# Kernel tuning notes

Measured on AMD Instinct MI355X. Metric: run time of the kernel, lower is better.

Reference implementation:

```python
import jax, jax.numpy as jnp
import numpy as np

N_S, N_D, E, L = 10000, 2000, 100000, 50000
H = 8            # attention heads
H1, H2, H3 = 128, 128, 64
D_S, D_D = 128, 64
NEG_SLOPE = 0.2  # GATv2 leaky_relu slope


def setup_inputs() -> dict:
    key = jax.random.key(0)
    ks = iter(jax.random.split(key, 48))
    def nrm(shape, fan_in):
        return (jax.random.normal(next(ks), shape) / np.sqrt(fan_in)).astype(jnp.float32)
    inp = {}
    inp["x_snorna"] = jax.random.normal(next(ks), (N_S, D_S), dtype=jnp.float32)
    inp["x_disease"] = jax.random.normal(next(ks), (N_D, D_D), dtype=jnp.float32)
    inp["edge_src"] = jax.random.randint(next(ks), (E,), 0, N_S, dtype=jnp.int32)
    inp["edge_dst"] = jax.random.randint(next(ks), (E,), 0, N_D, dtype=jnp.int32)
    inp["edge_label_src"] = jax.random.randint(next(ks), (L,), 0, N_S, dtype=jnp.int32)
    inp["edge_label_dst"] = jax.random.randint(next(ks), (L,), 0, N_D, dtype=jnp.int32)
    # layer 1: GraphConv per relation (lin_rel has bias, lin_root no bias)
    inp["W1_rel_sd"] = nrm((D_S, H1), D_S); inp["b1_sd"] = jnp.zeros((H1,), jnp.float32)
    inp["W1_root_sd"] = nrm((D_D, H1), D_D)
    inp["W1_rel_ds"] = nrm((D_D, H1), D_D); inp["b1_ds"] = jnp.zeros((H1,), jnp.float32)
    inp["W1_root_ds"] = nrm((D_S, H1), D_S)
    # layer 2: GATv2Conv per relation (lin_l/lin_r with bias, att, final bias)
    for rel in ("sd", "ds"):
        inp[f"Wl2_{rel}"] = nrm((H1, H * H2), H1); inp[f"bl2_{rel}"] = jnp.zeros((H * H2,), jnp.float32)
        inp[f"Wr2_{rel}"] = nrm((H1, H * H2), H1); inp[f"br2_{rel}"] = jnp.zeros((H * H2,), jnp.float32)
        inp[f"att2_{rel}"] = nrm((H, H2), H2)
        inp[f"bias2_{rel}"] = jnp.zeros((H2,), jnp.float32)
    # layer 3: GraphConv per relation
    inp["W3_rel_sd"] = nrm((H2, H3), H2); inp["b3_sd"] = jnp.zeros((H3,), jnp.float32)
    inp["W3_root_sd"] = nrm((H2, H3), H2)
    inp["W3_rel_ds"] = nrm((H2, H3), H2); inp["b3_ds"] = jnp.zeros((H3,), jnp.float32)
    inp["W3_root_ds"] = nrm((H2, H3), H2)
    return inp


def graph_conv(x_src, x_dst, es, ed, W_rel, b_rel, W_root, n_dst):
    # PyG GraphConv: lin_rel(sum-aggregated neighbor feats) + lin_root(x_dst)
    agg = jax.ops.segment_sum(x_src[es], ed, num_segments=n_dst)
    return agg @ W_rel + b_rel + x_dst @ W_root


def gatv2(x_src, x_dst, es, ed, Wl, bl, Wr, br, att, bias, n_dst):
    # PyG GATv2Conv, bipartite, add_self_loops=False, concat=False (mean over heads)
    xl = (x_src @ Wl + bl).reshape(x_src.shape[0], H, -1)  # [Ns,H,C]
    xr = (x_dst @ Wr + br).reshape(x_dst.shape[0], H, -1)  # [Nd,H,C]
    xj = xl[es]                                            # [E,H,C] source msgs
    e = jax.nn.leaky_relu(xj + xr[ed], NEG_SLOPE)          # [E,H,C]
    score = jnp.einsum('ehc,hc->eh', e, att)               # [E,H]
    m = jax.ops.segment_max(score, ed, num_segments=n_dst)
    a = jnp.exp(score - m[ed])
    denom = jax.ops.segment_sum(a, ed, num_segments=n_dst)
    alpha = a / denom[ed]                                  # softmax over in-edges of dst
    out = jax.ops.segment_sum(alpha[:, :, None] * xj, ed, num_segments=n_dst)
    return out.mean(axis=1) + bias                         # concat=False -> head mean


def reference(x_snorna, x_disease, edge_src, edge_dst, edge_label_src, edge_label_dst,
              W1_rel_sd, b1_sd, W1_root_sd, W1_rel_ds, b1_ds, W1_root_ds,
              Wl2_sd, bl2_sd, Wr2_sd, br2_sd, att2_sd, bias2_sd,
              Wl2_ds, bl2_ds, Wr2_ds, br2_ds, att2_ds, bias2_ds,
              W3_rel_sd, b3_sd, W3_root_sd, W3_rel_ds, b3_ds, W3_root_ds):
    # HeteroConv layer 1 (GraphConv both directions); each type has one incoming relation
    xd = graph_conv(x_snorna, x_disease, edge_src, edge_dst, W1_rel_sd, b1_sd, W1_root_sd, N_D)
    xs = graph_conv(x_disease, x_snorna, edge_dst, edge_src, W1_rel_ds, b1_ds, W1_root_ds, N_S)
    xs, xd = jax.nn.relu(xs), jax.nn.relu(xd)  # dropout = identity (eval mode)
    # HeteroConv layer 2 (GATv2Conv both directions)
    xd2 = gatv2(xs, xd, edge_src, edge_dst, Wl2_sd, bl2_sd, Wr2_sd, br2_sd, att2_sd, bias2_sd, N_D)
    xs2 = gatv2(xd, xs, edge_dst, edge_src, Wl2_ds, bl2_ds, Wr2_ds, br2_ds, att2_ds, bias2_ds, N_S)
    xs2, xd2 = jax.nn.relu(xs2), jax.nn.relu(xd2)
    # HeteroConv layer 3 (GraphConv, no activation)
    xd3 = graph_conv(xs2, xd2, edge_src, edge_dst, W3_rel_sd, b3_sd, W3_root_sd, N_D)
    xs3 = graph_conv(xd2, xs2, edge_dst, edge_src, W3_rel_ds, b3_ds, W3_root_ds, N_S)
    # Classifier: per-pair dot product
    return (xs3[edge_label_src] * xd3[edge_label_dst]).sum(axis=-1)
```

## Files before the change

### kernel.cpp

```cpp
#include <hip/hip_runtime.h>
#include <math.h>

#define HH 8
#define C2 128
#define NEG 0.2f

static const int N_S = 10000, N_D = 2000, E_N = 100000, L_N = 50000;

using short8 = __attribute__((ext_vector_type(8))) short;
using f32x4  = __attribute__((ext_vector_type(4))) float;

__device__ inline unsigned short f2bf(float f) {
  unsigned u = __float_as_uint(f);
  u += 0x7fff + ((u >> 16) & 1);
  return (unsigned short)(u >> 16);
}
__device__ inline float bf2f(unsigned short u) {
  return __uint_as_float((unsigned)u << 16);
}
__device__ inline void unpack16(uint4 u0, uint4 u1, float* x) {
  x[0]  = __uint_as_float(u0.x << 16); x[1]  = __uint_as_float(u0.x & 0xffff0000u);
  x[2]  = __uint_as_float(u0.y << 16); x[3]  = __uint_as_float(u0.y & 0xffff0000u);
  x[4]  = __uint_as_float(u0.z << 16); x[5]  = __uint_as_float(u0.z & 0xffff0000u);
  x[6]  = __uint_as_float(u0.w << 16); x[7]  = __uint_as_float(u0.w & 0xffff0000u);
  x[8]  = __uint_as_float(u1.x << 16); x[9]  = __uint_as_float(u1.x & 0xffff0000u);
  x[10] = __uint_as_float(u1.y << 16); x[11] = __uint_as_float(u1.y & 0xffff0000u);
  x[12] = __uint_as_float(u1.z << 16); x[13] = __uint_as_float(u1.z & 0xffff0000u);
  x[14] = __uint_as_float(u1.w << 16); x[15] = __uint_as_float(u1.w & 0xffff0000u);
}

__global__ void k_hist2(const int* __restrict__ es, const int* __restrict__ ed,
                        int* __restrict__ deg_s, int* __restrict__ deg_d, int E) {
  int e = blockIdx.x * 256 + threadIdx.x;
  if (e < E) {
    atomicAdd(&deg_d[ed[e]], 1);
    atomicAdd(&deg_s[es[e]], 1);
  }
}

__global__ __launch_bounds__(1024) void k_scan2(int* c0, int* r0, int n0,
                                                int* c1, int* r1, int n1) {
  int* cur = blockIdx.x ? c1 : c0;
  int* rp  = blockIdx.x ? r1 : r0;
  int N    = blockIdx.x ? n1 : n0;
  __shared__ int wsum[16];
  __shared__ int carry;
  if (threadIdx.x == 0) carry = 0;
  __syncthreads();
  int lane = threadIdx.x & 63, wid = threadIdx.x >> 6;
  for (int base = 0; base < N; base += 1024) {
    int i = base + threadIdx.x;
    int v = (i < N) ? cur[i] : 0;
    int x = v;
    #pragma unroll
    for (int dd = 1; dd < 64; dd <<= 1) {
      int t = __shfl_up(x, dd);
      if (lane >= dd) x += t;
    }
    if (lane == 63) wsum[wid] = x;
    __syncthreads();
    int woff = 0;
    for (int ww = 0; ww < wid; ++ww) woff += wsum[ww];
    int cl = carry;
    int excl = cl + woff + x - v;
    if (i < N) { rp[i] = excl; cur[i] = excl; }
    __syncthreads();
    if (threadIdx.x == 0) {
      int t = 0;
      #pragma unroll
      for (int ww = 0; ww < 16; ++ww) t += wsum[ww];
      if (base + 1024 >= N) rp[N] = carry + t;
      carry += t;
    }
    __syncthreads();
  }
}

__global__ void k_scat2(const int* __restrict__ es, const int* __restrict__ ed,
                        int* __restrict__ cur_d, int* __restrict__ cur_s,
                        int* __restrict__ csrc_d, int* __restrict__ csrc_s, int E) {
  int e = blockIdx.x * 256 + threadIdx.x;
  if (e >= E) return;
  int s = es[e], d = ed[e];
  csrc_d[atomicAdd(&cur_d[d], 1)] = s;
  csrc_s[atomicAdd(&cur_s[s], 1)] = d;
}

__global__ void k_cvt(const float* __restrict__ xs, const float* __restrict__ xd,
                      unsigned short* __restrict__ xsb, unsigned short* __restrict__ xdb) {
  int i = blockIdx.x * 256 + threadIdx.x;
  const int ns4 = N_S * 128 / 4, nd4 = N_D * 64 / 4;
  if (i < ns4) {
    float4 v = ((const float4*)xs)[i];
    ushort4 o = {f2bf(v.x), f2bf(v.y), f2bf(v.z), f2bf(v.w)};
    ((ushort4*)xsb)[i] = o;
  } else if (i < ns4 + nd4) {
    int j = i - ns4;
    float4 v = ((const float4*)xd)[j];
    ushort4 o = {f2bf(v.x), f2bf(v.y), f2bf(v.z), f2bf(v.w)};
    ((ushort4*)xdb)[j] = o;
  }
}

struct PkD { const float* W; unsigned short* P; int K, M; };
struct Pk12 { PkD d[12]; };
__global__ void k_pack(Pk12 g) {
  PkD d = g.d[blockIdx.y];
  int total = d.K * d.M;
  int mt = d.M >> 4;
  for (int tid = blockIdx.x * 256 + threadIdx.x; tid < total; tid += gridDim.x * 256) {
    int r = tid & 7, l = (tid >> 3) & 63;
    int rest = tid >> 9;
    int ct = rest % mt, kt = rest / mt;
    int k = kt * 32 + (l >> 4) * 8 + r;
    int col = ct * 16 + (l & 15);
    d.P[tid] = f2bf(d.W[k * d.M + col]);
  }
}

__global__ __launch_bounds__(128) void k_gather_l1(
    const unsigned short* __restrict__ xsb, const unsigned short* __restrict__ xdb,
    const int* __restrict__ rpd, const int* __restrict__ csd,
    const int* __restrict__ rps, const int* __restrict__ css,
    unsigned short* __restrict__ aggd, unsigned short* __restrict__ aggs) {
  if (blockIdx.x < N_D) {
    int n = blockIdx.x, c = threadIdx.x;
    int b = rpd[n], e = rpd[n + 1];
    float acc = 0.f;
    int i = b;
    for (; i + 1 < e; i += 2)
      acc += bf2f(xsb[(long long)csd[i] * 128 + c]) +
             bf2f(xsb[(long long)csd[i + 1] * 128 + c]);
    if (i < e) acc += bf2f(xsb[(long long)csd[i] * 128 + c]);
    aggd[(long long)n * 128 + c] = f2bf(acc);
  } else {
    int n = (blockIdx.x - N_D) * 2 + (threadIdx.x >> 6);
    int c = threadIdx.x & 63;
    if (n >= N_S) return;
    int b = rps[n], e = rps[n + 1];
    float acc = 0.f;
    int i = b;
    for (; i + 1 < e; i += 2)
      acc += bf2f(xdb[(long long)css[i] * 64 + c]) +
             bf2f(xdb[(long long)css[i + 1] * 64 + c]);
    if (i < e) acc += bf2f(xdb[(long long)css[i] * 64 + c]);
    aggs[(long long)n * 64 + c] = f2bf(acc);
  }
}

__global__ __launch_bounds__(128) void k_gather_l3(
    const unsigned short* __restrict__ xs2b, const unsigned short* __restrict__ xd2b,
    const int* __restrict__ rpd, const int* __restrict__ csd,
    const int* __restrict__ rps, const int* __restrict__ css,
    unsigned short* __restrict__ aggd, unsigned short* __restrict__ aggs) {
  int c = threadIdx.x;
  if (blockIdx.x < N_D) {
    int n = blockIdx.x;
    int b = rpd[n], e = rpd[n + 1];
    float acc = 0.f;
    int i = b;
    for (; i + 1 < e; i += 2)
      acc += bf2f(xs2b[(long long)csd[i] * 128 + c]) +
             bf2f(xs2b[(long long)csd[i + 1] * 128 + c]);
    if (i < e) acc += bf2f(xs2b[(long long)csd[i] * 128 + c]);
    aggd[(long long)n * 128 + c] = f2bf(acc);
  } else {
    int n = blockIdx.x - N_D;
    int b = rps[n], e = rps[n + 1];
    float acc = 0.f;
    int i = b;
    for (; i + 1 < e; i += 2)
      acc += bf2f(xd2b[(long long)css[i] * 128 + c]) +
             bf2f(xd2b[(long long)css[i + 1] * 128 + c]);
    if (i < e) acc += bf2f(xd2b[(long long)css[i] * 128 + c]);
    aggs[(long long)n * 128 + c] = f2bf(acc);
  }
}

struct GD {
  const unsigned short *A0, *P0, *A1, *P1;
  const float* bias;
  void* out;
  int K0, K1, N, M, relu, outbf, y0;
};
template<int ND> struct GDs { GD d[ND]; };

template<int ND>
__global__ __launch_bounds__(256) void k_mfma(GDs<ND> g) {
  int by = blockIdx.y;
  int di = 0;
  #pragma unroll
  for (int i = 1; i < ND; ++i) if (by >= g.d[i].y0) di = i;
  GD d = g.d[di];
  int ytile = by - d.y0;
  int c0 = blockIdx.x * 64;
  if (c0 >= d.M) return;
  int w = threadIdx.x >> 6, l = threadIdx.x & 63;
  int r0 = ytile * 64 + w * 16;
  if (r0 >= d.N) return;
  int lg = l >> 4, lo = l & 15;
  f32x4 acc[4] = {};
  int arow = r0 + lo; arow = (arow < d.N) ? arow : (d.N - 1);
  int mt = d.M >> 4;
  int ct0 = c0 >> 4;
  const unsigned short* a0 = d.A0 + (long long)arow * d.K0 + lg * 8;
  for (int kt = 0; kt < (d.K0 >> 5); ++kt) {
    short8 a = *(const short8*)(a0 + kt * 32);
    #pragma unroll
    for (int ct = 0; ct < 4; ++ct) {
      short8 b = *(const short8*)(d.P0 + ((long long)(kt * mt + ct0 + ct) * 64 + l) * 8);
      acc[ct] = __builtin_amdgcn_mfma_f32_16x16x32_bf16(a, b, acc[ct], 0, 0, 0);
    }
  }
  if (d.K1) {
    const unsigned short* a1 = d.A1 + (long long)arow * d.K1 + lg * 8;
    for (int kt = 0; kt < (d.K1 >> 5); ++kt) {
      short8 a = *(const short8*)(a1 + kt * 32);
      #pragma unroll
      for (int ct = 0; ct < 4; ++ct) {
        short8 b = *(const short8*)(d.P1 + ((long long)(kt * mt + ct0 + ct) * 64 + l) * 8);
        acc[ct] = __builtin_amdgcn_mfma_f32_16x16x32_bf16(a, b, acc[ct], 0, 0, 0);
      }
    }
  }
  #pragma unroll
  for (int ct = 0; ct < 4; ++ct) {
    int col = c0 + ct * 16 + lo;
    float bv = d.bias[col];
    #pragma unroll
    for (int r = 0; r < 4; ++r) {
      int grow = r0 + lg * 4 + r;
      if (grow < d.N) {
        float v = acc[ct][r] + bv;
        if (d.relu) v = fmaxf(v, 0.f);
        if (d.outbf)
          ((unsigned short*)d.out)[(long long)grow * d.M + col] = f2bf(v);
        else
          ((float*)d.out)[(long long)grow * d.M + col] = v;
      }
    }
  }
}

template<int WPN>
__device__ __forceinline__ void gat_node(
    const unsigned short* __restrict__ xl, const unsigned short* __restrict__ xr,
    const int* __restrict__ rowptr, const int* __restrict__ srcid,
    const float* __restrict__ att, const float* __restrict__ bias,
    unsigned short* __restrict__ outb, int node, int wsub, int l,
    float (*lm)[8], float (*lss)[8], float (*lacc)[64][16]) {
  int h = l >> 3, sub = l & 7;
  int cbase = h * 128 + sub * 16;

  float xrv[16], atv[16];
  {
    const uint4* p = (const uint4*)(xr + (long long)node * 1024 + cbase);
    unpack16(p[0], p[1], xrv);
    const float4* pa = (const float4*)(att + cbase);
    float4 a0 = pa[0], a1 = pa[1], a2 = pa[2], a3 = pa[3];
    atv[0] = a0.x; atv[1] = a0.y; atv[2] = a0.z; atv[3] = a0.w;
    atv[4] = a1.x; atv[5] = a1.y; atv[6] = a1.z; atv[7] = a1.w;
    atv[8] = a2.x; atv[9] = a2.y; atv[10] = a2.z; atv[11] = a2.w;
    atv[12] = a3.x; atv[13] = a3.y; atv[14] = a3.z; atv[15] = a3.w;
  }

  float m = -INFINITY, s = 0.f, acc[16] = {};
  int b = rowptr[node], e = rowptr[node + 1];

  auto process = [&](uint4 u0, uint4 u1) {
    float x[16];
    unpack16(u0, u1, x);
    float sc = 0.f;
    #pragma unroll
    for (int j = 0; j < 16; ++j) {
      float t = x[j] + xrv[j];
      t = fmaxf(t, NEG * t);
      sc = fmaf(t, atv[j], sc);
    }
    sc += __shfl_xor(sc, 1); sc += __shfl_xor(sc, 2); sc += __shfl_xor(sc, 4);
    if (sc > m + 8.f) {
      float scl = __expf(m - sc);
      s *= scl;
      #pragma unroll
      for (int j = 0; j < 16; ++j) acc[j] *= scl;
      m = sc;
    }
    float a = __expf(sc - m);
    s += a;
    #pragma unroll
    for (int j = 0; j < 16; ++j) acc[j] = fmaf(a, x[j], acc[j]);
  };

  int i = b + wsub;
  uint4 c0, c1, d0, d1;
  bool hc = (i < e), hd = (i + WPN < e);
  if (hc) { const uint4* p = (const uint4*)(xl + (long long)srcid[i] * 1024 + cbase); c0 = p[0]; c1 = p[1]; }
  if (hd) { const uint4* p = (const uint4*)(xl + (long long)srcid[i + WPN] * 1024 + cbase); d0 = p[0]; d1 = p[1]; }
  while (hc) {
    int inx = i + 2 * WPN;
    uint4 n0, n1, n2, n3;
    bool h0 = (inx < e), h1 = (inx + WPN < e);
    if (h0) { const uint4* p = (const uint4*)(xl + (long long)srcid[inx] * 1024 + cbase); n0 = p[0]; n1 = p[1]; }
    if (h1) { const uint4* p = (const uint4*)(xl + (long long)srcid[inx + WPN] * 1024 + cbase); n2 = p[0]; n3 = p[1]; }
    process(c0, c1);
    if (hd) process(d0, d1);
    c0 = n0; c1 = n1; d0 = n2; d1 = n3;
    hc = h0; hd = h1;
    i = inx;
  }

  float val[16];
  if constexpr (WPN == 4) {
    if (sub == 0) { lm[wsub][h] = m; lss[wsub][h] = s; }
    #pragma unroll
    for (int q = 0; q < 4; ++q) {
      float4 t = {acc[q * 4], acc[q * 4 + 1], acc[q * 4 + 2], acc[q * 4 + 3]};
      *(float4*)&lacc[wsub][l][q * 4] = t;
    }
    __syncthreads();
    if (wsub != 0) return;
    float M2 = fmaxf(fmaxf(lm[0][h], lm[1][h]), fmaxf(lm[2][h], lm[3][h]));
    float S = 0.f;
    #pragma unroll
    for (int j = 0; j < 16; ++j) val[j] = 0.f;
    #pragma unroll
    for (int w2 = 0; w2 < 4; ++w2) {
      float scw = (M2 == -INFINITY) ? 0.f : __expf(lm[w2][h] - M2);
      S = fmaf(scw, lss[w2][h], S);
      #pragma unroll
      for (int j = 0; j < 16; ++j) val[j] = fmaf(scw, lacc[w2][l][j], val[j]);
    }
    float inv = (S > 0.f) ? 1.f / S : 0.f;
    #pragma unroll
    for (int j = 0; j < 16; ++j) val[j] *= inv;
  } else {
    float inv = (s > 0.f) ? 1.f / s : 0.f;
    #pragma unroll
    for (int j = 0; j < 16; ++j) val[j] = acc[j] * inv;
  }
  #pragma unroll
  for (int j = 0; j < 16; ++j) {
    val[j] += __shfl_xor(val[j], 8);
    val[j] += __shfl_xor(val[j], 16);
    val[j] += __shfl_xor(val[j], 32);
  }
  if (l < 8) {
    #pragma unroll
    for (int q = 0; q < 4; ++q) {
      float4 bq = *(const float4*)&bias[sub * 16 + q * 4];
      ushort4 o;
      o.x = f2bf(fmaxf(val[q * 4 + 0] * 0.125f + bq.x, 0.f));
      o.y = f2bf(fmaxf(val[q * 4 + 1] * 0.125f + bq.y, 0.f));
      o.z = f2bf(fmaxf(val[q * 4 + 2] * 0.125f + bq.z, 0.f));
      o.w = f2bf(fmaxf(val[q * 4 + 3] * 0.125f + bq.w, 0.f));
      *(ushort4*)&outb[(long long)node * C2 + sub * 16 + q * 4] = o;
    }
  }
}

__global__ __launch_bounds__(256) void k_gat_both(
    const unsigned short* __restrict__ XLsd, const unsigned short* __restrict__ XRsd,
    const int* __restrict__ rpd, const int* __restrict__ csd,
    const float* __restrict__ att_sd, const float* __restrict__ bias_sd,
    unsigned short* __restrict__ XD2b,
    const unsigned short* __restrict__ XLds, const unsigned short* __restrict__ XRds,
    const int* __restrict__ rps, const int* __restrict__ css,
    const float* __restrict__ att_ds, const float* __restrict__ bias_ds,
    unsigned short* __restrict__ XS2b) {
  __shared__ float lm[4][8], lss[4][8];
  __shared__ float lacc[4][64][16];
  int widx = threadIdx.x >> 6, l = threadIdx.x & 63;
  if (blockIdx.x < (unsigned)N_D) {
    gat_node<4>(XLsd, XRsd, rpd, csd, att_sd, bias_sd, XD2b,
                blockIdx.x, widx, l, lm, lss, lacc);
  } else {
    int node = (blockIdx.x - N_D) * 4 + widx;
    if (node < N_S)
      gat_node<1>(XLds, XRds, rps, css, att_ds, bias_ds, XS2b,
                  node, 0, l, lm, lss, lacc);
  }
}

__global__ void k_dot64(const float* __restrict__ xs, const float* __restrict__ xd,
                        const int* __restrict__ ls, const int* __restrict__ ld,
                        float* __restrict__ out, int L) {
  long long t = (long long)blockIdx.x * blockDim.x + threadIdx.x;
  int wave = (int)(t >> 6), lane = (int)(t & 63);
  int q = lane >> 4, sub = lane & 15;
  int eidx = wave * 4 + q;
  if (eidx >= L) return;
  const float4* a = (const float4*)(xs + (long long)ls[eidx] * 64);
  const float4* b = (const float4*)(xd + (long long)ld[eidx] * 64);
  float4 va = a[sub], vb = b[sub];
  float v = va.x * vb.x + va.y * vb.y + va.z * vb.z + va.w * vb.w;
  v += __shfl_xor(v, 1); v += __shfl_xor(v, 2);
  v += __shfl_xor(v, 4); v += __shfl_xor(v, 8);
  if (sub == 0) out[eidx] = v;
}

extern "C" void kernel_launch(void* const* d_in, const int* in_sizes, int n_in,
                              void* d_out, int out_size, void* d_ws, size_t ws_size,
                              hipStream_t stream) {
  const float* x_s = (const float*)d_in[0];
  const float* x_d = (const float*)d_in[1];
  const int* esrc = (const int*)d_in[2];
  const int* edst = (const int*)d_in[3];
  const int* lsrc = (const int*)d_in[4];
  const int* ldst = (const int*)d_in[5];
  const float* W1rel_sd  = (const float*)d_in[6];
  const float* b1_sd     = (const float*)d_in[7];
  const float* W1root_sd = (const float*)d_in[8];
  const float* W1rel_ds  = (const float*)d_in[9];
  const float* b1_ds     = (const float*)d_in[10];
  const float* W1root_ds = (const float*)d_in[11];
  const float *Wl2_sd = (const float*)d_in[12], *bl2_sd = (const float*)d_in[13],
              *Wr2_sd = (const float*)d_in[14], *br2_sd = (const float*)d_in[15],
              *att2_sd = (const float*)d_in[16], *bias2_sd = (const float*)d_in[17];
  const float *Wl2_ds = (const float*)d_in[18], *bl2_ds = (const float*)d_in[19],
              *Wr2_ds = (const float*)d_in[20], *br2_ds = (const float*)d_in[21],
              *att2_ds = (const float*)d_in[22], *bias2_ds = (const float*)d_in[23];
  const float *W3rel_sd = (const float*)d_in[24], *b3_sd = (const float*)d_in[25],
              *W3root_sd = (const float*)d_in[26];
  const float *W3rel_ds = (const float*)d_in[27], *b3_ds = (const float*)d_in[28],
              *W3root_ds = (const float*)d_in[29];
  float* out = (float*)d_out;

  float* w = (float*)d_ws;
  long long off = 0;
  auto alloc = [&](long long n) { float* p = w + off; off += (n + 63) & ~63LL; return p; };
  unsigned short* xsb   = (unsigned short*)alloc((long long)N_S * 64);
  unsigned short* xdb   = (unsigned short*)alloc((long long)N_D * 32);
  unsigned short* AGGDb = (unsigned short*)alloc((long long)N_D * 64);
  unsigned short* AGGSb = (unsigned short*)alloc((long long)N_S * 32);
  unsigned short* XS1b  = (unsigned short*)alloc((long long)N_S * 64);
  unsigned short* XD1b  = (unsigned short*)alloc((long long)N_D * 64);
  unsigned short* XLsd  = (unsigned short*)alloc((long long)N_S * 512);
  unsigned short* XRsd  = (unsigned short*)alloc((long long)N_D * 512);
  unsigned short* XLds  = (unsigned short*)alloc((long long)N_D * 512);
  unsigned short* XRds  = (unsigned short*)alloc((long long)N_S * 512);
  unsigned short* XS2b  = (unsigned short*)alloc((long long)N_S * 64);
  unsigned short* XD2b  = (unsigned short*)alloc((long long)N_D * 64);
  unsigned short* AGD3b = (unsigned short*)alloc((long long)N_D * 64);
  unsigned short* AGS3b = (unsigned short*)alloc((long long)N_S * 64);
  float* XS3 = alloc((long long)N_S * 64);
  float* XD3 = alloc((long long)N_D * 64);
  unsigned short* pk[12];
  const int pksz[12] = {128 * 128, 64 * 128, 64 * 128, 128 * 128,
                        131072, 131072, 131072, 131072,
                        128 * 64, 128 * 64, 128 * 64, 128 * 64};
  for (int i = 0; i < 12; ++i) pk[i] = (unsigned short*)alloc(pksz[i] / 2 + 64);
  int* rowptr_d = (int*)alloc(N_D + 64);
  int* rowptr_s = (int*)alloc(N_S + 64);
  int* cur_all  = (int*)alloc(N_D + N_S + 128);
  int* cur_d = cur_all;
  int* cur_s = cur_all + N_D + 64;
  int* csrc_d = (int*)alloc(E_N);
  int* csrc_s = (int*)alloc(E_N);
  (void)ws_size; (void)in_sizes; (void)n_in; (void)out_size;

  k_cvt<<<(N_S * 32 + N_D * 16 + 255) / 256, 256, 0, stream>>>(x_s, x_d, xsb, xdb);
  Pk12 pkk = {{{W1rel_sd, pk[0], 128, 128}, {W1root_sd, pk[1], 64, 128},
               {W1rel_ds, pk[2], 64, 128},  {W1root_ds, pk[3], 128, 128},
               {Wl2_sd, pk[4], 128, 1024},  {Wr2_sd, pk[5], 128, 1024},
               {Wl2_ds, pk[6], 128, 1024},  {Wr2_ds, pk[7], 128, 1024},
               {W3rel_sd, pk[8], 128, 64},  {W3root_sd, pk[9], 128, 64},
               {W3rel_ds, pk[10], 128, 64}, {W3root_ds, pk[11], 128, 64}}};
  k_pack<<<dim3(64, 12), 256, 0, stream>>>(pkk);

  hipMemsetAsync(cur_all, 0, (size_t)(N_D + N_S + 128) * 4, stream);
  k_hist2<<<(E_N + 255) / 256, 256, 0, stream>>>(esrc, edst, cur_s, cur_d, E_N);
  k_scan2<<<2, 1024, 0, stream>>>(cur_d, rowptr_d, N_D, cur_s, rowptr_s, N_S);
  k_scat2<<<(E_N + 255) / 256, 256, 0, stream>>>(esrc, edst, cur_d, cur_s,
                                                 csrc_d, csrc_s, E_N);

  k_gather_l1<<<N_D + (N_S + 1) / 2, 128, 0, stream>>>(
      xsb, xdb, rowptr_d, csrc_d, rowptr_s, csrc_s, AGGDb, AGGSb);
  {
    GDs<2> g = {{{AGGDb, pk[0], xdb, pk[1], b1_sd, XD1b, 128, 64, N_D, 128, 1, 1, 0},
                 {AGGSb, pk[2], xsb, pk[3], b1_ds, XS1b, 64, 128, N_S, 128, 1, 1, 32}}};
    k_mfma<2><<<dim3(2, 189), 256, 0, stream>>>(g);
  }

  {
    GDs<4> g = {{{XS1b, pk[4], nullptr, nullptr, bl2_sd, XLsd, 128, 0, N_S, 1024, 0, 1, 0},
                 {XD1b, pk[5], nullptr, nullptr, br2_sd, XRsd, 128, 0, N_D, 1024, 0, 1, 157},
                 {XD1b, pk[6], nullptr, nullptr, bl2_ds, XLds, 128, 0, N_D, 1024, 0, 1, 189},
                 {XS1b, pk[7], nullptr, nullptr, br2_ds, XRds, 128, 0, N_S, 1024, 0, 1, 221}}};
    k_mfma<4><<<dim3(16, 378), 256, 0, stream>>>(g);
  }
  k_gat_both<<<N_D + (N_S + 3) / 4, 256, 0, stream>>>(
      XLsd, XRsd, rowptr_d, csrc_d, att2_sd, bias2_sd, XD2b,
      XLds, XRds, rowptr_s, csrc_s, att2_ds, bias2_ds, XS2b);

  k_gather_l3<<<N_D + N_S, 128, 0, stream>>>(
      XS2b, XD2b, rowptr_d, csrc_d, rowptr_s, csrc_s, AGD3b, AGS3b);
  {
    GDs<2> g = {{{AGD3b, pk[8], XD2b, pk[9], b3_sd, XD3, 128, 128, N_D, 64, 0, 0, 0},
                 {AGS3b, pk[10], XS2b, pk[11], b3_ds, XS3, 128, 128, N_S, 64, 0, 0, 32}}};
    k_mfma<2><<<dim3(1, 189), 256, 0, stream>>>(g);
  }

  k_dot64<<<(L_N * 16 + 255) / 256, 256, 0, stream>>>(XS3, XD3, lsrc, ldst, out, L_N);
}
```

Measured before the change: 210.8 us.

## Use packed fp16 GATv2 math, merge prep kernels, vectorize neighbor gathers

The GATv2 projection GEMMs now write fp16 instead of bf16. The attention kernel computes leaky-relu scores with packed half2 ops and fdot2, and accumulates messages in half2 with a 1/256 pre-scale. Histogram, input conversion, weight packing and attention-vector conversion are merged into one prep launch to cut launch overhead. The layer-1 and layer-3 gathers become one wave per node, with vectorized loads split across two half-waves. Together these aim to cut ALU work, LDS footprint and launch count, at the cost of reduced accumulation precision and a tighter rescale threshold in the online softmax.

```diff
diff --git a/kernel.cpp b/kernel.cpp
--- a/kernel.cpp
+++ b/kernel.cpp
@@ -1,14 +1,14 @@
 #include <hip/hip_runtime.h>
 #include <math.h>
 
-#define HH 8
-#define C2 128
 #define NEG 0.2f
-
 static const int N_S = 10000, N_D = 2000, E_N = 100000, L_N = 50000;
 
 using short8 = __attribute__((ext_vector_type(8))) short;
 using f32x4  = __attribute__((ext_vector_type(4))) float;
+typedef _Float16 h2 __attribute__((ext_vector_type(2)));
+
+union U8h { uint4 u[2]; h2 h[8]; unsigned w[8]; };
 
 __device__ inline unsigned short f2bf(float f) {
   unsigned u = __float_as_uint(f);
@@ -18,23 +18,57 @@
 __device__ inline float bf2f(unsigned short u) {
   return __uint_as_float((unsigned)u << 16);
 }
-__device__ inline void unpack16(uint4 u0, uint4 u1, float* x) {
-  x[0]  = __uint_as_float(u0.x << 16); x[1]  = __uint_as_float(u0.x & 0xffff0000u);
-  x[2]  = __uint_as_float(u0.y << 16); x[3]  = __uint_as_float(u0.y & 0xffff0000u);
-  x[4]  = __uint_as_float(u0.z << 16); x[5]  = __uint_as_float(u0.z & 0xffff0000u);
-  x[6]  = __uint_as_float(u0.w << 16); x[7]  = __uint_as_float(u0.w & 0xffff0000u);
-  x[8]  = __uint_as_float(u1.x << 16); x[9]  = __uint_as_float(u1.x & 0xffff0000u);
-  x[10] = __uint_as_float(u1.y << 16); x[11] = __uint_as_float(u1.y & 0xffff0000u);
-  x[12] = __uint_as_float(u1.z << 16); x[13] = __uint_as_float(u1.z & 0xffff0000u);
-  x[14] = __uint_as_float(u1.w << 16); x[15] = __uint_as_float(u1.w & 0xffff0000u);
-}
-
-__global__ void k_hist2(const int* __restrict__ es, const int* __restrict__ ed,
-                        int* __restrict__ deg_s, int* __restrict__ deg_d, int E) {
-  int e = blockIdx.x * 256 + threadIdx.x;
-  if (e < E) {
-    atomicAdd(&deg_d[ed[e]], 1);
-    atomicAdd(&deg_s[es[e]], 1);
+__device__ inline unsigned short f2h(float f) {
+  _Float16 h = (_Float16)f;
+  unsigned short r;
+  __builtin_memcpy(&r, &h, 2);
+  return r;
+}
+
+struct PkD { const float* W; unsigned short* P; int K, M; };
+struct Pk12 { PkD d[12]; };
+struct PrepArgs {
+  const int *es, *ed;
+  int *deg_s, *deg_d;
+  const float *xs, *xd;
+  unsigned short *xsb, *xdb;
+  const float *att_sd, *att_ds;
+  unsigned short *att16;
+};
+__global__ void k_prep(PrepArgs a, Pk12 g) {
+  int bid = blockIdx.x, t = threadIdx.x;
+  if (bid < 391) {
+    int e = bid * 256 + t;
+    if (e < E_N) {
+      atomicAdd(&a.deg_d[a.ed[e]], 1);
+      atomicAdd(&a.deg_s[a.es[e]], 1);
+    }
+  } else if (bid < 391 + 1375) {
+    int i = (bid - 391) * 256 + t;
+    const int ns4 = N_S * 32;
+    if (i < ns4) {
+      float4 v = ((const float4*)a.xs)[i];
+      ushort4 o = {f2bf(v.x), f2bf(v.y), f2bf(v.z), f2bf(v.w)};
+      ((ushort4*)a.xsb)[i] = o;
+    } else {
+      int j = i - ns4;
+      float4 v = ((const float4*)a.xd)[j];
+      ushort4 o = {f2bf(v.x), f2bf(v.y), f2bf(v.z), f2bf(v.w)};
+      ((ushort4*)a.xdb)[j] = o;
+    }
+  } else if (bid < 391 + 1375 + 768) {
+    int sub = bid - 391 - 1375;
+    PkD d = g.d[sub >> 6];
+    int total = d.K * d.M, mt = d.M >> 4;
+    for (int tid = (sub & 63) * 256 + t; tid < total; tid += 64 * 256) {
+      int r = tid & 7, l = (tid >> 3) & 63, rest = tid >> 9;
+      int ct = rest % mt, kt = rest / mt;
+      d.P[tid] = f2bf(d.W[(kt * 32 + (l >> 4) * 8 + r) * d.M + ct * 16 + (l & 15)]);
+    }
+  } else {
+    int i = (bid - 391 - 1375 - 768) * 256 + t;
+    float v = (i < 1024) ? a.att_sd[i] : a.att_ds[i - 1024];
+    a.att16[i] = f2h(v);
   }
 }
 
@@ -61,8 +95,7 @@
     __syncthreads();
     int woff = 0;
     for (int ww = 0; ww < wid; ++ww) woff += wsum[ww];
-    int cl = carry;
-    int excl = cl + woff + x - v;
+    int excl = carry + woff + x - v;
     if (i < N) { rp[i] = excl; cur[i] = excl; }
     __syncthreads();
     if (threadIdx.x == 0) {
@@ -86,94 +119,83 @@
   csrc_s[atomicAdd(&cur_s[s], 1)] = d;
 }
 
-__global__ void k_cvt(const float* __restrict__ xs, const float* __restrict__ xd,
-                      unsigned short* __restrict__ xsb, unsigned short* __restrict__ xdb) {
-  int i = blockIdx.x * 256 + threadIdx.x;
-  const int ns4 = N_S * 128 / 4, nd4 = N_D * 64 / 4;
-  if (i < ns4) {
-    float4 v = ((const float4*)xs)[i];
-    ushort4 o = {f2bf(v.x), f2bf(v.y), f2bf(v.z), f2bf(v.w)};
-    ((ushort4*)xsb)[i] = o;
-  } else if (i < ns4 + nd4) {
-    int j = i - ns4;
-    float4 v = ((const float4*)xd)[j];
-    ushort4 o = {f2bf(v.x), f2bf(v.y), f2bf(v.z), f2bf(v.w)};
-    ((ushort4*)xdb)[j] = o;
-  }
-}
-
-struct PkD { const float* W; unsigned short* P; int K, M; };
-struct Pk12 { PkD d[12]; };
-__global__ void k_pack(Pk12 g) {
-  PkD d = g.d[blockIdx.y];
-  int total = d.K * d.M;
-  int mt = d.M >> 4;
-  for (int tid = blockIdx.x * 256 + threadIdx.x; tid < total; tid += gridDim.x * 256) {
-    int r = tid & 7, l = (tid >> 3) & 63;
-    int rest = tid >> 9;
-    int ct = rest % mt, kt = rest / mt;
-    int k = kt * 32 + (l >> 4) * 8 + r;
-    int col = ct * 16 + (l & 15);
-    d.P[tid] = f2bf(d.W[k * d.M + col]);
-  }
-}
-
-__global__ __launch_bounds__(128) void k_gather_l1(
+__device__ __forceinline__ void gath128(const unsigned short* __restrict__ x,
+                                        const int* __restrict__ rp, const int* __restrict__ cs,
+                                        unsigned short* __restrict__ out,
+                                        int n, int half, int cl) {
+  int b = rp[n], e = rp[n + 1];
+  float a0 = 0.f, a1 = 0.f, a2 = 0.f, a3 = 0.f;
+  int i = b + half;
+  for (; i + 2 < e; i += 4) {
+    uint2 v0 = *(const uint2*)(x + (long long)cs[i] * 128 + cl * 4);
+    uint2 v1 = *(const uint2*)(x + (long long)cs[i + 2] * 128 + cl * 4);
+    a0 += bf2f((unsigned short)(v0.x & 0xffff)) + bf2f((unsigned short)(v1.x & 0xffff));
+    a1 += bf2f((unsigned short)(v0.x >> 16))    + bf2f((unsigned short)(v1.x >> 16));
+    a2 += bf2f((unsigned short)(v0.y & 0xffff)) + bf2f((unsigned short)(v1.y & 0xffff));
+    a3 += bf2f((unsigned short)(v0.y >> 16))    + bf2f((unsigned short)(v1.y >> 16));
+  }
+  for (; i < e; i += 2) {
+    uint2 v0 = *(const uint2*)(x + (long long)cs[i] * 128 + cl * 4);
+    a0 += bf2f((unsigned short)(v0.x & 0xffff));
+    a1 += bf2f((unsigned short)(v0.x >> 16));
+    a2 += bf2f((unsigned short)(v0.y & 0xffff));
+    a3 += bf2f((unsigned short)(v0.y >> 16));
+  }
+  a0 += __shfl_xor(a0, 32); a1 += __shfl_xor(a1, 32);
+  a2 += __shfl_xor(a2, 32); a3 += __shfl_xor(a3, 32);
+  if (!half) {
+    ushort4 o = {f2bf(a0), f2bf(a1), f2bf(a2), f2bf(a3)};
+    *(ushort4*)&out[(long long)n * 128 + cl * 4] = o;
+  }
+}
+
+__global__ __launch_bounds__(256) void k_gather1(
     const unsigned short* __restrict__ xsb, const unsigned short* __restrict__ xdb,
     const int* __restrict__ rpd, const int* __restrict__ csd,
     const int* __restrict__ rps, const int* __restrict__ css,
     unsigned short* __restrict__ aggd, unsigned short* __restrict__ aggs) {
-  if (blockIdx.x < N_D) {
-    int n = blockIdx.x, c = threadIdx.x;
-    int b = rpd[n], e = rpd[n + 1];
-    float acc = 0.f;
-    int i = b;
-    for (; i + 1 < e; i += 2)
-      acc += bf2f(xsb[(long long)csd[i] * 128 + c]) +
-             bf2f(xsb[(long long)csd[i + 1] * 128 + c]);
-    if (i < e) acc += bf2f(xsb[(long long)csd[i] * 128 + c]);
-    aggd[(long long)n * 128 + c] = f2bf(acc);
+  int wv = threadIdx.x >> 6, l = threadIdx.x & 63, half = l >> 5, cl = l & 31;
+  int bid = blockIdx.x;
+  if (bid < 500) {
+    gath128(xsb, rpd, csd, aggd, bid * 4 + wv, half, cl);
   } else {
-    int n = (blockIdx.x - N_D) * 2 + (threadIdx.x >> 6);
-    int c = threadIdx.x & 63;
+    int n = (bid - 500) * 4 + wv;
     if (n >= N_S) return;
     int b = rps[n], e = rps[n + 1];
-    float acc = 0.f;
-    int i = b;
-    for (; i + 1 < e; i += 2)
-      acc += bf2f(xdb[(long long)css[i] * 64 + c]) +
-             bf2f(xdb[(long long)css[i + 1] * 64 + c]);
-    if (i < e) acc += bf2f(xdb[(long long)css[i] * 64 + c]);
-    aggs[(long long)n * 64 + c] = f2bf(acc);
-  }
-}
-
-__global__ __launch_bounds__(128) void k_gather_l3(
+    float a0 = 0.f, a1 = 0.f;
+    int i = b + half;
+    for (; i + 2 < e; i += 4) {
+      unsigned v0 = *(const unsigned*)(xdb + (long long)css[i] * 64 + cl * 2);
+      unsigned v1 = *(const unsigned*)(xdb + (long long)css[i + 2] * 64 + cl * 2);
+      a0 += bf2f((unsigned short)(v0 & 0xffff)) + bf2f((unsigned short)(v1 & 0xffff));
+      a1 += bf2f((unsigned short)(v0 >> 16))    + bf2f((unsigned short)(v1 >> 16));
+    }
+    for (; i < e; i += 2) {
+      unsigned v0 = *(const unsigned*)(xdb + (long long)css[i] * 64 + cl * 2);
+      a0 += bf2f((unsigned short)(v0 & 0xffff));
+      a1 += bf2f((unsigned short)(v0 >> 16));
+    }
+    a0 += __shfl_xor(a0, 32); a1 += __shfl_xor(a1, 32);
+    if (!half) {
+      ushort2 o = {f2bf(a0), f2bf(a1)};
+      *(ushort2*)&aggs[(long long)n * 64 + cl * 2] = o;
+    }
+  }
+}
+
+__global__ __launch_bounds__(256) void k_gather3(
     const unsigned short* __restrict__ xs2b, const unsigned short* __restrict__ xd2b,
     const int* __restrict__ rpd, const int* __restrict__ csd,
     const int* __restrict__ rps, const int* __restrict__ css,
     unsigned short* __restrict__ aggd, unsigned short* __restrict__ aggs) {
-  int c = threadIdx.x;
-  if (blockIdx.x < N_D) {
-    int n = blockIdx.x;
-    int b = rpd[n], e = rpd[n + 1];
-    float acc = 0.f;
-    int i = b;
-    for (; i + 1 < e; i += 2)
-      acc += bf2f(xs2b[(long long)csd[i] * 128 + c]) +
-             bf2f(xs2b[(long long)csd[i + 1] * 128 + c]);
-    if (i < e) acc += bf2f(xs2b[(long long)csd[i] * 128 + c]);
-    aggd[(long long)n * 128 + c] = f2bf(acc);
+  int wv = threadIdx.x >> 6, l = threadIdx.x & 63, half = l >> 5, cl = l & 31;
+  int bid = blockIdx.x;
+  if (bid < 500) {
+    gath128(xs2b, rpd, csd, aggd, bid * 4 + wv, half, cl);
   } else {
-    int n = blockIdx.x - N_D;
-    int b = rps[n], e = rps[n + 1];
-    float acc = 0.f;
-    int i = b;
-    for (; i + 1 < e; i += 2)
-      acc += bf2f(xd2b[(long long)css[i] * 128 + c]) +
-             bf2f(xd2b[(long long)css[i + 1] * 128 + c]);
-    if (i < e) acc += bf2f(xd2b[(long long)css[i] * 128 + c]);
-    aggs[(long long)n * 128 + c] = f2bf(acc);
+    int n = (bid - 500) * 4 + wv;
+    if (n >= N_S) return;
+    gath128(xd2b, rps, css, aggs, n, half, cl);
   }
 }
 
@@ -181,7 +203,7 @@
   const unsigned short *A0, *P0, *A1, *P1;
   const float* bias;
   void* out;
-  int K0, K1, N, M, relu, outbf, y0;
+  int K0, K1, N, M, relu, outmode, y0;
 };
 template<int ND> struct GDs { GD d[ND]; };
 
@@ -233,8 +255,10 @@
       if (grow < d.N) {
         float v = acc[ct][r] + bv;
         if (d.relu) v = fmaxf(v, 0.f);
-        if (d.outbf)
+        if (d.outmode == 1)
           ((unsigned short*)d.out)[(long long)grow * d.M + col] = f2bf(v);
+        else if (d.outmode == 2)
+          ((unsigned short*)d.out)[(long long)grow * d.M + col] = f2h(v);
         else
           ((float*)d.out)[(long long)grow * d.M + col] = v;
       }
@@ -246,77 +270,70 @@
 __device__ __forceinline__ void gat_node(
     const unsigned short* __restrict__ xl, const unsigned short* __restrict__ xr,
     const int* __restrict__ rowptr, const int* __restrict__ srcid,
-    const float* __restrict__ att, const float* __restrict__ bias,
+    const unsigned short* __restrict__ att16, const float* __restrict__ bias,
     unsigned short* __restrict__ outb, int node, int wsub, int l,
-    float (*lm)[8], float (*lss)[8], float (*lacc)[64][16]) {
+    float (*lm)[8], float (*lss)[8], unsigned (*lacc)[8][64]) {
   int h = l >> 3, sub = l & 7;
   int cbase = h * 128 + sub * 16;
-
-  float xrv[16], atv[16];
-  {
-    const uint4* p = (const uint4*)(xr + (long long)node * 1024 + cbase);
-    unpack16(p[0], p[1], xrv);
-    const float4* pa = (const float4*)(att + cbase);
-    float4 a0 = pa[0], a1 = pa[1], a2 = pa[2], a3 = pa[3];
-    atv[0] = a0.x; atv[1] = a0.y; atv[2] = a0.z; atv[3] = a0.w;
-    atv[4] = a1.x; atv[5] = a1.y; atv[6] = a1.z; atv[7] = a1.w;
-    atv[8] = a2.x; atv[9] = a2.y; atv[10] = a2.z; atv[11] = a2.w;
-    atv[12] = a3.x; atv[13] = a3.y; atv[14] = a3.z; atv[15] = a3.w;
-  }
-
-  float m = -INFINITY, s = 0.f, acc[16] = {};
+  U8h xr8, at8;
+  { const uint4* p = (const uint4*)(xr + (long long)node * 1024 + cbase);
+    xr8.u[0] = p[0]; xr8.u[1] = p[1]; }
+  { const uint4* p = (const uint4*)(att16 + cbase);
+    at8.u[0] = p[0]; at8.u[1] = p[1]; }
+  const h2 neg2 = {(_Float16)NEG, (_Float16)NEG};
+  float m = -INFINITY, s = 0.f;
+  h2 acc2[8] = {};
   int b = rowptr[node], e = rowptr[node + 1];
 
-  auto process = [&](uint4 u0, uint4 u1) {
-    float x[16];
-    unpack16(u0, u1, x);
+  auto process = [&](U8h& x) {
     float sc = 0.f;
     #pragma unroll
-    for (int j = 0; j < 16; ++j) {
-      float t = x[j] + xrv[j];
-      t = fmaxf(t, NEG * t);
-      sc = fmaf(t, atv[j], sc);
+    for (int j = 0; j < 8; ++j) {
+      h2 t = x.h[j] + xr8.h[j];
+      h2 lk = __builtin_elementwise_max(t, t * neg2);
+      sc = __builtin_amdgcn_fdot2(lk, at8.h[j], sc, false);
     }
     sc += __shfl_xor(sc, 1); sc += __shfl_xor(sc, 2); sc += __shfl_xor(sc, 4);
-    if (sc > m + 8.f) {
+    if (sc > m + 4.f) {
       float scl = __expf(m - sc);
-      s *= scl;
+      _Float16 sh = (_Float16)scl;
+      h2 s2 = {sh, sh};
       #pragma unroll
-      for (int j = 0; j < 16; ++j) acc[j] *= scl;
-      m = sc;
+      for (int j = 0; j < 8; ++j) acc2[j] *= s2;
+      s *= scl; m = sc;
     }
     float a = __expf(sc - m);
     s += a;
-    #pragma unroll
-    for (int j = 0; j < 16; ++j) acc[j] = fmaf(a, x[j], acc[j]);
+    _Float16 ah = (_Float16)(a * 0.00390625f);
+    h2 a2 = {ah, ah};
+    #pragma unroll
+    for (int j = 0; j < 8; ++j) acc2[j] = __builtin_elementwise_fma(a2, x.h[j], acc2[j]);
   };
 
   int i = b + wsub;
-  uint4 c0, c1, d0, d1;
+  U8h c, d;
   bool hc = (i < e), hd = (i + WPN < e);
-  if (hc) { const uint4* p = (const uint4*)(xl + (long long)srcid[i] * 1024 + cbase); c0 = p[0]; c1 = p[1]; }
-  if (hd) { const uint4* p = (const uint4*)(xl + (long long)srcid[i + WPN] * 1024 + cbase); d0 = p[0]; d1 = p[1]; }
+  if (hc) { const uint4* p = (const uint4*)(xl + (long long)srcid[i] * 1024 + cbase); c.u[0] = p[0]; c.u[1] = p[1]; }
+  if (hd) { const uint4* p = (const uint4*)(xl + (long long)srcid[i + WPN] * 1024 + cbase); d.u[0] = p[0]; d.u[1] = p[1]; }
   while (hc) {
     int inx = i + 2 * WPN;
-    uint4 n0, n1, n2, n3;
+    U8h n0, n1;
     bool h0 = (inx < e), h1 = (inx + WPN < e);
-    if (h0) { const uint4* p = (const uint4*)(xl + (long long)srcid[inx] * 1024 + cbase); n0 = p[0]; n1 = p[1]; }
-    if (h1) { const uint4* p = (const uint4*)(xl + (long long)srcid[inx + WPN] * 1024 + cbase); n2 = p[0]; n3 = p[1]; }
-    process(c0, c1);
-    if (hd) process(d0, d1);
-    c0 = n0; c1 = n1; d0 = n2; d1 = n3;
-    hc = h0; hd = h1;
-    i = inx;
+    if (h0) { const uint4* p = (const uint4*)(xl + (long long)srcid[inx] * 1024 + cbase); n0.u[0] = p[0]; n0.u[1] = p[1]; }
+    if (h1) { const uint4* p = (const uint4*)(xl + (long long)srcid[inx + WPN] * 1024 + cbase); n1.u[0] = p[0]; n1.u[1] = p[1]; }
+    process(c);
+    if (hd) process(d);
+    c = n0; d = n1; hc = h0; hd = h1; i = inx;
   }
 
   float val[16];
   if constexpr (WPN == 4) {
     if (sub == 0) { lm[wsub][h] = m; lss[wsub][h] = s; }
-    #pragma unroll
-    for (int q = 0; q < 4; ++q) {
-      float4 t = {acc[q * 4], acc[q * 4 + 1], acc[q * 4 + 2], acc[q * 4 + 3]};
-      *(float4*)&lacc[wsub][l][q * 4] = t;
-    }
+    U8h tmp;
+    #pragma unroll
+    for (int j = 0; j < 8; ++j) tmp.h[j] = acc2[j];
+    #pragma unroll
+    for (int j = 0; j < 8; ++j) lacc[wsub][j][l] = tmp.w[j];
     __syncthreads();
     if (wsub != 0) return;
     float M2 = fmaxf(fmaxf(lm[0][h], lm[1][h]), fmaxf(lm[2][h], lm[3][h]));
@@ -328,15 +345,23 @@
       float scw = (M2 == -INFINITY) ? 0.f : __expf(lm[w2][h] - M2);
       S = fmaf(scw, lss[w2][h], S);
       #pragma unroll
-      for (int j = 0; j < 16; ++j) val[j] = fmaf(scw, lacc[w2][l][j], val[j]);
-    }
-    float inv = (S > 0.f) ? 1.f / S : 0.f;
+      for (int j = 0; j < 8; ++j) {
+        unsigned uw = lacc[w2][j][l];
+        h2 hv; __builtin_memcpy(&hv, &uw, 4);
+        val[2 * j]     = fmaf(scw, (float)hv[0], val[2 * j]);
+        val[2 * j + 1] = fmaf(scw, (float)hv[1], val[2 * j + 1]);
+      }
+    }
+    float inv = (S > 0.f) ? 256.f / S : 0.f;
     #pragma unroll
     for (int j = 0; j < 16; ++j) val[j] *= inv;
   } else {
-    float inv = (s > 0.f) ? 1.f / s : 0.f;
-    #pragma unroll
-    for (int j = 0; j < 16; ++j) val[j] = acc[j] * inv;
+    float inv = (s > 0.f) ? 256.f / s : 0.f;
+    #pragma unroll
+    for (int j = 0; j < 8; ++j) {
+      val[2 * j]     = (float)acc2[j][0] * inv;
+      val[2 * j + 1] = (float)acc2[j][1] * inv;
+    }
   }
   #pragma unroll
   for (int j = 0; j < 16; ++j) {
@@ -353,7 +378,7 @@
       o.y = f2bf(fmaxf(val[q * 4 + 1] * 0.125f + bq.y, 0.f));
       o.z = f2bf(fmaxf(val[q * 4 + 2] * 0.125f + bq.z, 0.f));
       o.w = f2bf(fmaxf(val[q * 4 + 3] * 0.125f + bq.w, 0.f));
-      *(ushort4*)&outb[(long long)node * C2 + sub * 16 + q * 4] = o;
+      *(ushort4*)&outb[(long long)node * 128 + sub * 16 + q * 4] = o;
     }
   }
 }
@@ -361,14 +386,14 @@
 __global__ __launch_bounds__(256) void k_gat_both(
     const unsigned short* __restrict__ XLsd, const unsigned short* __restrict__ XRsd,
     const int* __restrict__ rpd, const int* __restrict__ csd,
-    const float* __restrict__ att_sd, const float* __restrict__ bias_sd,
+    const unsigned short* __restrict__ att_sd, const float* __restrict__ bias_sd,
     unsigned short* __restrict__ XD2b,
     const unsigned short* __restrict__ XLds, const unsigned short* __restrict__ XRds,
     const int* __restrict__ rps, const int* __restrict__ css,
-    const float* __restrict__ att_ds, const float* __restrict__ bias_ds,
+    const unsigned short* __restrict__ att_ds, const float* __restrict__ bias_ds,
     unsigned short* __restrict__ XS2b) {
   __shared__ float lm[4][8], lss[4][8];
-  __shared__ float lacc[4][64][16];
+  __shared__ unsigned lacc[4][8][64];
   int widx = threadIdx.x >> 6, l = threadIdx.x & 63;
   if (blockIdx.x < (unsigned)N_D) {
     gat_node<4>(XLsd, XRsd, rpd, csd, att_sd, bias_sd, XD2b,
@@ -444,6 +469,7 @@
   unsigned short* AGS3b = (unsigned short*)alloc((long long)N_S * 64);
   float* XS3 = alloc((long long)N_S * 64);
   float* XD3 = alloc((long long)N_D * 64);
+  unsigned short* att16 = (unsigned short*)alloc(1024 + 64);
   unsigned short* pk[12];
   const int pksz[12] = {128 * 128, 64 * 128, 64 * 128, 128 * 128,
                         131072, 131072, 131072, 131072,
@@ -458,23 +484,20 @@
   int* csrc_s = (int*)alloc(E_N);
   (void)ws_size; (void)in_sizes; (void)n_in; (void)out_size;
 
-  k_cvt<<<(N_S * 32 + N_D * 16 + 255) / 256, 256, 0, stream>>>(x_s, x_d, xsb, xdb);
+  hipMemsetAsync(cur_all, 0, (size_t)(N_D + N_S + 128) * 4, stream);
+  PrepArgs pa = {esrc, edst, cur_s, cur_d, x_s, x_d, xsb, xdb, att2_sd, att2_ds, att16};
   Pk12 pkk = {{{W1rel_sd, pk[0], 128, 128}, {W1root_sd, pk[1], 64, 128},
                {W1rel_ds, pk[2], 64, 128},  {W1root_ds, pk[3], 128, 128},
                {Wl2_sd, pk[4], 128, 1024},  {Wr2_sd, pk[5], 128, 1024},
                {Wl2_ds, pk[6], 128, 1024},  {Wr2_ds, pk[7], 128, 1024},
                {W3rel_sd, pk[8], 128, 64},  {W3root_sd, pk[9], 128, 64},
                {W3rel_ds, pk[10], 128, 64}, {W3root_ds, pk[11], 128, 64}}};
-  k_pack<<<dim3(64, 12), 256, 0, stream>>>(pkk);
-
-  hipMemsetAsync(cur_all, 0, (size_t)(N_D + N_S + 128) * 4, stream);
-  k_hist2<<<(E_N + 255) / 256, 256, 0, stream>>>(esrc, edst, cur_s, cur_d, E_N);
+  k_prep<<<2542, 256, 0, stream>>>(pa, pkk);
   k_scan2<<<2, 1024, 0, stream>>>(cur_d, rowptr_d, N_D, cur_s, rowptr_s, N_S);
-  k_scat2<<<(E_N + 255) / 256, 256, 0, stream>>>(esrc, edst, cur_d, cur_s,
-                                                 csrc_d, csrc_s, E_N);
-
-  k_gather_l1<<<N_D + (N_S + 1) / 2, 128, 0, stream>>>(
-      xsb, xdb, rowptr_d, csrc_d, rowptr_s, csrc_s, AGGDb, AGGSb);
+  k_scat2<<<391, 256, 0, stream>>>(esrc, edst, cur_d, cur_s, csrc_d, csrc_s, E_N);
+
+  k_gather1<<<3000, 256, 0, stream>>>(xsb, xdb, rowptr_d, csrc_d, rowptr_s, csrc_s,
+                                      AGGDb, AGGSb);
   {
     GDs<2> g = {{{AGGDb, pk[0], xdb, pk[1], b1_sd, XD1b, 128, 64, N_D, 128, 1, 1, 0},
                  {AGGSb, pk[2], xsb, pk[3], b1_ds, XS1b, 64, 128, N_S, 128, 1, 1, 32}}};
@@ -482,18 +505,18 @@
   }
 
   {
-    GDs<4> g = {{{XS1b, pk[4], nullptr, nullptr, bl2_sd, XLsd, 128, 0, N_S, 1024, 0, 1, 0},
-                 {XD1b, pk[5], nullptr, nullptr, br2_sd, XRsd, 128, 0, N_D, 1024, 0, 1, 157},
-                 {XD1b, pk[6], nullptr, nullptr, bl2_ds, XLds, 128, 0, N_D, 1024, 0, 1, 189},
-                 {XS1b, pk[7], nullptr, nullptr, br2_ds, XRds, 128, 0, N_S, 1024, 0, 1, 221}}};
+    GDs<4> g = {{{XS1b, pk[4], nullptr, nullptr, bl2_sd, XLsd, 128, 0, N_S, 1024, 0, 2, 0},
+                 {XD1b, pk[5], nullptr, nullptr, br2_sd, XRsd, 128, 0, N_D, 1024, 0, 2, 157},
+                 {XD1b, pk[6], nullptr, nullptr, bl2_ds, XLds, 128, 0, N_D, 1024, 0, 2, 189},
+                 {XS1b, pk[7], nullptr, nullptr, br2_ds, XRds, 128, 0, N_S, 1024, 0, 2, 221}}};
     k_mfma<4><<<dim3(16, 378), 256, 0, stream>>>(g);
   }
   k_gat_both<<<N_D + (N_S + 3) / 4, 256, 0, stream>>>(
-      XLsd, XRsd, rowptr_d, csrc_d, att2_sd, bias2_sd, XD2b,
-      XLds, XRds, rowptr_s, csrc_s, att2_ds, bias2_ds, XS2b);
-
-  k_gather_l3<<<N_D + N_S, 128, 0, stream>>>(
-      XS2b, XD2b, rowptr_d, csrc_d, rowptr_s, csrc_s, AGD3b, AGS3b);
+      XLsd, XRsd, rowptr_d, csrc_d, att16, bias2_sd, XD2b,
+      XLds, XRds, rowptr_s, csrc_s, att16 + 1024, bias2_ds, XS2b);
+
+  k_gather3<<<3000, 256, 0, stream>>>(XS2b, XD2b, rowptr_d, csrc_d, rowptr_s, csrc_s,
+                                      AGD3b, AGS3b);
   {
     GDs<2> g = {{{AGD3b, pk[8], XD2b, pk[9], b3_sd, XD3, 128, 128, N_D, 64, 0, 0, 0},
                  {AGS3b, pk[10], XS2b, pk[11], b3_ds, XS3, 128, 128, N_S, 64, 0, 0, 32}}};
```

New measurement: 199.8 us (median of 2 runs). -5.2%, faster.
